# Kernel tuning notes

Measured on AMD Instinct MI355X. Metric: run time of the kernel, lower is better.

Reference implementation:

```python
import jax, jax.numpy as jnp
import numpy as np
from itertools import combinations

NUM_LAGS = 9
WINDOWS = 4
HIDDEN = 256
BS = 32768
EPS = 1e-5  # BatchNorm eps


def _mean_adj():
    # Reconstruct the fixed per-sample DGL graph from get_batch_graph and
    # fold mean-aggregation into a row-normalized dense 9x9 matrix
    # (duplicate edges across overlapping windows count with multiplicity,
    # exactly as DGL's mailbox mean does).
    edges = []
    for j in range(WINDOWS, NUM_LAGS + 1):
        t = list(range(j - WINDOWS, j))
        combs = list(combinations(t, 2))
        for e in combs[:-1]:  # code drops the last combination per window
            edges.append(e)
    edges.append((NUM_LAGS - 2, NUM_LAGS - 1))
    edges.append((NUM_LAGS - 1, 0))
    A = np.zeros((NUM_LAGS, NUM_LAGS), np.float32)
    for s, d in edges:
        A[d, s] += 1.0  # messages flow src -> dst
    deg = A.sum(axis=1, keepdims=True)
    return A / np.maximum(deg, 1.0)

_A = jnp.asarray(_mean_adj())  # [9, 9]


def setup_inputs() -> dict:
    key = jax.random.key(0)
    ks = jax.random.split(key, 12)
    H = HIDDEN
    s = lambda fan_in: 1.0 / np.sqrt(fan_in)
    return {
        "lags": jax.random.normal(ks[0], (BS, NUM_LAGS), jnp.float32),
        "weather": jax.random.normal(ks[1], (BS, NUM_LAGS, 8), jnp.float32),
        "W_l1": jax.random.normal(ks[2], (1, H), jnp.float32) * s(1),
        "b_l1": jnp.zeros((H,), jnp.float32),
        "g_bn": jnp.ones((H,), jnp.float32),
        "b_bn": jnp.zeros((H,), jnp.float32),
        "W_l2": jax.random.normal(ks[3], (H, H), jnp.float32) * s(H),
        "b_l2": jnp.zeros((H,), jnp.float32),
        "W_w1": jax.random.normal(ks[4], (8, H), jnp.float32) * s(8),
        "b_w1": jnp.zeros((H,), jnp.float32),
        "W_w2": jax.random.normal(ks[5], (H, H), jnp.float32) * s(H),
        "b_w2": jnp.zeros((H,), jnp.float32),
        "Wm1": jax.random.normal(ks[6], (2 * H, H), jnp.float32) * s(2 * H),
        "bm1": jnp.zeros((H,), jnp.float32),
        "Wm2": jax.random.normal(ks[7], (2 * H, H), jnp.float32) * s(2 * H),
        "bm2": jnp.zeros((H,), jnp.float32),
        "W_reg": jax.random.normal(ks[8], (NUM_LAGS * H, 1), jnp.float32) * s(NUM_LAGS * H),
        "b_reg": jnp.zeros((1,), jnp.float32),
    }


def reference(lags, weather, W_l1, b_l1, g_bn, b_bn, W_l2, b_l2,
              W_w1, b_w1, W_w2, b_w2, Wm1, bm1, Wm2, bm2, W_reg, b_reg):
    bs = lags.shape[0]
    # lags branch: Linear(1,H) -> tanh -> [dropout=id] -> eval BatchNorm -> Linear(H,H) -> tanh
    l = jnp.tanh(lags.reshape(-1, 1) @ W_l1 + b_l1)
    l = l * (g_bn / jnp.sqrt(1.0 + EPS)) + b_bn  # BN eval: running_mean=0, running_var=1
    l = jnp.tanh(l @ W_l2 + b_l2)
    # weather branch: Linear(8,H) -> tanh -> Linear(H,H) -> tanh
    w = jnp.tanh(weather.reshape(-1, 8) @ W_w1 + b_w1)
    w = jnp.tanh(w @ W_w2 + b_w2)
    l = l.reshape(bs, NUM_LAGS, -1)
    w = w.reshape(bs, NUM_LAGS, -1)
    # Two MGN layers: mean-aggregate neighbor l and w, concat, linear merge.
    for Wm, bm in ((Wm1, bm1), (Wm2, bm2)):
        ml = jnp.einsum('ds,bsh->bdh', _A, l)  # mean over mailbox 'l'
        mw = jnp.einsum('ds,bsh->bdh', _A, w)  # mean over mailbox 'w'
        l = jnp.concatenate([ml, mw], axis=-1) @ Wm + bm
        w = mw
    hg = l.reshape(bs, -1)  # [bs, 9*H]
    return hg @ W_reg + b_reg
```

## Files before the change

### kernel.cpp

```cpp
#include <hip/hip_runtime.h>

typedef __attribute__((ext_vector_type(8))) short short8;
typedef __attribute__((ext_vector_type(4))) float float4v;

#define NLAGS 9
#define HID 256
#define GSAMP 16
#define NTHREADS 512
#define SBUF_SHORTS (36864 + 256 + 288)

#define NK 2048
#define LUT_STRIDE 2056
#define SLO -8.0f
#define KINV 128.0f

union S8 { short8 v; unsigned short u[8]; };

__device__ __forceinline__ unsigned short f2b(float f) {
  union { float f; unsigned int i; } c; c.f = f;
  return (unsigned short)((c.i + 0x7FFFu + ((c.i >> 16) & 1u)) >> 16);
}
__device__ __forceinline__ float sane(float x) {
  return (__builtin_isfinite(x) && fabsf(x) < 1e30f) ? x : 0.0f;
}
__device__ __forceinline__ unsigned int pkbf16(float lo, float hi) {
  unsigned int r;
  asm("v_cvt_pk_bf16_f32 %0, %1, %2" : "=v"(r) : "v"(lo), "v"(hi));
  return r;
}
__device__ __forceinline__ float ftanh(float x) {
  float t = __expf(2.0f * x);
  return 1.0f - 2.0f * __builtin_amdgcn_rcpf(t + 1.0f);
}
__device__ __forceinline__ float4v mfma16(short8 a, short8 b, float4v c) {
  return __builtin_amdgcn_mfma_f32_16x16x32_bf16(a, b, c, 0, 0, 0);
}

__device__ __forceinline__ int tmC(int row, int c) {
  int base = ((row >> 4) * 8 + (c >> 2)) * 512 + (row & 15) * 32 + (c & 3) * 8;
  return base ^ ((((c >> 2) ^ (row >> 2)) & 3) << 4);
}
__device__ __forceinline__ int tmE(int row, int col) {
  int base = ((row >> 4) * 8 + (col >> 5)) * 512 + (row & 15) * 32 + (col & 31);
  return base ^ ((((col >> 5) ^ (row >> 2)) & 3) << 4);
}

#define A_TABLE { \
    {0,0,0,0,0,0,0,0,1}, \
    {1,0,0,0,0,0,0,0,0}, \
    {1.f/3,2.f/3,0,0,0,0,0,0,0}, \
    {0.2f,0.4f,0.4f,0,0,0,0,0,0}, \
    {0,0.2f,0.4f,0.4f,0,0,0,0,0}, \
    {0,0,0.2f,0.4f,0.4f,0,0,0,0}, \
    {0,0,0,0.2f,0.4f,0.4f,0,0,0}, \
    {0,0,0,0,0.25f,0.5f,0.25f,0,0}, \
    {0,0,0,0,0,1.f/3,1.f/3,1.f/3,0}, \
  }

__global__ void prep_all(const float* __restrict__ Ww2,
                         const float* __restrict__ Ww1,
                         const float* __restrict__ Wm2,
                         const float* __restrict__ Wreg,
                         const float* __restrict__ bm2,
                         const float* __restrict__ breg,
                         unsigned short* __restrict__ ws,
                         float* __restrict__ vtab)
{
  const int b = blockIdx.x;
  if (b < 144) {
    int idx = b * 512 + threadIdx.x + 65536;
    if (idx < 131072) {
      int j = idx - 65536; int n = j >> 8, k = j & 255;
      ws[idx] = f2b(sane(Ww2[k * 256 + n]));
    } else {
      int j = idx - 131072; int n = j >> 5, k = j & 31;
      ws[idx] = (k < 8) ? f2b(sane(Ww1[k * 256 + n])) : (unsigned short)0;
    }
    return;
  }
  const float A[9][9] = A_TABLE;
  const int lane = threadIdx.x & 63;
  const int g = (b - 144) * 8 + (threadIdx.x >> 6);
  if (g < 4608) {
    int mat = (g >= 2304);
    int w = g - mat * 2304;
    int d = w >> 8, k = w & 255;
    float coef[9];
    #pragma unroll
    for (int dp = 0; dp < 9; ++dp) {
      if (!mat) {
        coef[dp] = A[dp][d];
      } else {
        float s = 0.f;
        #pragma unroll
        for (int e = 0; e < 9; ++e) s += A[dp][e] * A[e][d];
        coef[dp] = s;
      }
    }
    const float* wm2row = Wm2 + (size_t)(mat * 256 + k) * 256;
    float acc = 0.f;
    #pragma unroll
    for (int it = 0; it < 4; ++it) {
      int h = lane + it * 64;
      float wp = 0.f;
      #pragma unroll
      for (int dp = 0; dp < 9; ++dp) wp = fmaf(coef[dp], Wreg[dp * 256 + h], wp);
      acc = fmaf(wp, wm2row[h], acc);
    }
    #pragma unroll
    for (int off = 32; off >= 1; off >>= 1) acc += __shfl_down(acc, off);
    if (lane == 0) vtab[5120 + g] = acc;
  } else if (g == 4608) {
    float c0 = 0.f;
    #pragma unroll
    for (int it = 0; it < 4; ++it) {
      int h = lane + it * 64;
      float cs = 0.f;
      #pragma unroll
      for (int d = 0; d < 9; ++d) cs += Wreg[d * 256 + h];
      c0 = fmaf(bm2[h], cs, c0);
    }
    #pragma unroll
    for (int off = 32; off >= 1; off >>= 1) c0 += __shfl_down(c0, off);
    if (lane == 0) vtab[9728] = c0 + breg[0];
  }
}

__global__ void prep2b_kernel(const float* __restrict__ Wm1,
                              const float* __restrict__ bm1,
                              float* __restrict__ vtab)
{
  const float A[9][9] = A_TABLE;
  const float* V1s = vtab + 5120;
  const float* V2s = vtab + 7424;
  const int lane = threadIdx.x & 63;
  const int g = blockIdx.x * 8 + (threadIdx.x >> 6);
  if (g < 4608) {
    int mat = (g >= 2304);
    int w = g - mat * 2304;
    int s = w >> 8, k = w & 255;
    const float* wm1row = Wm1 + (size_t)(mat * 256 + k) * 256;
    float acc = 0.f;
    #pragma unroll
    for (int it = 0; it < 4; ++it) {
      int h = lane + it * 64;
      float u = 0.f;
      #pragma unroll
      for (int d = 0; d < 9; ++d) u = fmaf(A[d][s], V1s[d * 256 + h], u);
      acc = fmaf(u, wm1row[h], acc);
    }
    #pragma unroll
    for (int off = 32; off >= 1; off >>= 1) acc += __shfl_down(acc, off);
    if (lane == 0) vtab[g] = acc + (mat ? V2s[s * 256 + k] : 0.f);
  } else if (g == 4608) {
    float c = 0.f;
    #pragma unroll
    for (int it = 0; it < 4; ++it) {
      int h = lane + it * 64;
      float vs = 0.f;
      #pragma unroll
      for (int d = 0; d < 9; ++d) vs += V1s[d * 256 + h];
      c = fmaf(bm1[h], vs, c);
    }
    #pragma unroll
    for (int off = 32; off >= 1; off >>= 1) c += __shfl_down(c, off);
    if (lane == 0) vtab[4608] = c + vtab[9728];
  }
}

__global__ void prep3_lut(const float* __restrict__ Wl1,
                          const float* __restrict__ bl1,
                          const float* __restrict__ gbn,
                          const float* __restrict__ bbn,
                          const float* __restrict__ Wl2,
                          const float* __restrict__ bl2,
                          const float* __restrict__ vtab,
                          float* __restrict__ lutf)
{
  __shared__ float l0s[2][256];
  __shared__ float red[2][9][4];
  const int tid = threadIdx.x;
  const int b = blockIdx.x;
  const float BNS = 0.99999500003750f;
  {
    float w = Wl1[tid], a = bl1[tid], g = gbn[tid] * BNS, q = bbn[tid];
    #pragma unroll
    for (int j = 0; j < 2; ++j) {
      float s = SLO + (float)(b * 2 + j) * 0.0078125f;
      l0s[j][tid] = fmaf(ftanh(fmaf(s, w, a)), g, q);
    }
  }
  __syncthreads();
  float z0 = bl2[tid], z1 = z0;
  #pragma unroll 8
  for (int k = 0; k < 256; ++k) {
    float wv = Wl2[k * 256 + tid];
    z0 = fmaf(l0s[0][k], wv, z0);
    z1 = fmaf(l0s[1][k], wv, z1);
  }
  float t0 = ftanh(z0), t1 = ftanh(z1);
  const int lane = tid & 63, w4 = tid >> 6;
  for (int d = 0; d < 9; ++d) {
    float T1h = vtab[d * 256 + tid];
    float v0 = t0 * T1h, v1 = t1 * T1h;
    #pragma unroll
    for (int off = 32; off >= 1; off >>= 1) {
      v0 += __shfl_down(v0, off);
      v1 += __shfl_down(v1, off);
    }
    if (lane == 0) { red[0][d][w4] = v0; red[1][d][w4] = v1; }
  }
  __syncthreads();
  if (tid < 18) {
    int j = tid / 9, d = tid - j * 9;
    float v = red[j][d][0] + red[j][d][1] + red[j][d][2] + red[j][d][3];
    lutf[d * LUT_STRIDE + (b * 2 + j)] = v;
  }
}

__global__ void __launch_bounds__(NTHREADS, 2)
fused_kernel(const float* __restrict__ lags,
             const float* __restrict__ weather,
             const float* __restrict__ bw1,
             const float* __restrict__ bw2,
             const unsigned short* __restrict__ ws,
             const float* __restrict__ vtab,
             float* __restrict__ out)
{
  __shared__ __align__(16) unsigned short sBuf[SBUF_SHORTS];
  unsigned short* sT = sBuf;
  float* scratch  = (float*)(sBuf + 36864);
  float* scratch2 = (float*)(sBuf + 36864 + 256);

  const int tid = threadIdx.x;
  const int wave = tid >> 6;
  const int lane16 = tid & 15;
  const int g4 = (tid >> 4) & 3;
  const int s0 = blockIdx.x * GSAMP;

  const float* lutf = (const float*)ws;
  const unsigned short* Ww2t = ws + 65536;
  const unsigned short* Ww1p = ws + 131072;

  const int c0 = wave * 32 + lane16;
  const int c1 = wave * 32 + 16 + lane16;

  if (tid < 144) {
    int samp = tid / 9, d = tid - samp * 9;
    float x = lags[(s0 + samp) * NLAGS + d];
    float tp = (x - SLO) * KINV;
    tp = fminf(fmaxf(tp, 0.0f), (float)(NK - 2) + 0.999f);
    int j = (int)tp; float fr = tp - (float)j;
    const float* row = lutf + d * LUT_STRIDE;
    float lo = row[j], hi = row[j + 1];
    scratch2[tid] = fmaf(fr, hi - lo, lo);
  }

  {
    short8 bf0 = *(const short8*)(Ww1p + c0 * 32 + g4 * 8);
    short8 bf1 = *(const short8*)(Ww1p + c1 * 32 + g4 * 8);
    float bia0 = bw1[c0], bia1 = bw1[c1];
    #pragma unroll
    for (int m = 0; m < 9; ++m) {
      S8 a8;
      if (g4 == 0) {
        const float* wp = weather + (size_t)(s0 + lane16) * 72 + m * 8;
        float4v x0 = *(const float4v*)(wp);
        float4v x1 = *(const float4v*)(wp + 4);
        a8.v = (short8){0,0,0,0,0,0,0,0};
        unsigned int p0 = pkbf16(x0[0], x0[1]), p1 = pkbf16(x0[2], x0[3]);
        unsigned int p2 = pkbf16(x1[0], x1[1]), p3 = pkbf16(x1[2], x1[3]);
        a8.u[0] = (unsigned short)p0; a8.u[1] = (unsigned short)(p0 >> 16);
        a8.u[2] = (unsigned short)p1; a8.u[3] = (unsigned short)(p1 >> 16);
        a8.u[4] = (unsigned short)p2; a8.u[5] = (unsigned short)(p2 >> 16);
        a8.u[6] = (unsigned short)p3; a8.u[7] = (unsigned short)(p3 >> 16);
      } else {
        a8.v = (short8){0,0,0,0,0,0,0,0};
      }
      float4v zz = {0.f, 0.f, 0.f, 0.f};
      float4v ac0 = mfma16(a8.v, bf0, zz);
      float4v ac1 = mfma16(a8.v, bf1, zz);
      #pragma unroll
      for (int i = 0; i < 4; ++i) {
        int row = m * 16 + g4 * 4 + i;
        unsigned int p = pkbf16(ftanh(ac0[i] + bia0), ftanh(ac1[i] + bia1));
        sT[tmE(row, c0)] = (unsigned short)p;
        sT[tmE(row, c1)] = (unsigned short)(p >> 16);
      }
    }
  }
  __syncthreads();

  float P[4] = {0.f, 0.f, 0.f, 0.f};

  {
    float4v acc0[9], acc1[9];
    #pragma unroll
    for (int m = 0; m < 9; ++m) {
      float4v z = {0.f,0.f,0.f,0.f};
      acc0[m] = z; acc1[m] = z;
    }
    #pragma unroll
    for (int kk = 0; kk < 8; ++kk) {
      short8 b0 = *(const short8*)(Ww2t + c0 * 256 + kk * 32 + g4 * 8);
      short8 b1 = *(const short8*)(Ww2t + c1 * 256 + kk * 32 + g4 * 8);
      #pragma unroll
      for (int m = 0; m < 9; ++m) {
        short8 a = *(const short8*)(sT + tmC(m * 16 + lane16, kk * 4 + g4));
        acc0[m] = mfma16(a, b0, acc0[m]);
        acc1[m] = mfma16(a, b1, acc1[m]);
      }
    }
    float twc0[9], twc1[9];
    #pragma unroll
    for (int m = 0; m < 9; ++m) {
      twc0[m] = vtab[2304 + m * 256 + c0];
      twc1[m] = vtab[2304 + m * 256 + c1];
    }
    float bia0 = bw2[c0], bia1 = bw2[c1];
    #pragma unroll
    for (int m = 0; m < 9; ++m) {
      #pragma unroll
      for (int i = 0; i < 4; ++i) {
        float t0 = ftanh(acc0[m][i] + bia0);
        float t1 = ftanh(acc1[m][i] + bia1);
        P[i] = fmaf(t0, twc0[m], P[i]);
        P[i] = fmaf(t1, twc1[m], P[i]);
      }
    }
  }

  #pragma unroll
  for (int off = 8; off >= 1; off >>= 1) {
    #pragma unroll
    for (int i = 0; i < 4; ++i) P[i] += __shfl_down(P[i], off, 16);
  }
  if (lane16 == 0) {
    #pragma unroll
    for (int i = 0; i < 4; ++i) scratch[wave * 16 + g4 * 4 + i] = P[i];
  }
  __syncthreads();
  if (tid < GSAMP) {
    float sum = 0.f;
    #pragma unroll
    for (int w = 0; w < 8; ++w) sum += scratch[w * 16 + tid];
    float lsum = 0.f;
    #pragma unroll
    for (int d = 0; d < 9; ++d) lsum += scratch2[tid * 9 + d];
    out[s0 + tid] = sum + lsum + vtab[4608];
  }
}

extern "C" void kernel_launch(void* const* d_in, const int* in_sizes, int n_in,
                              void* d_out, int out_size, void* d_ws, size_t ws_size,
                              hipStream_t stream) {
  const float* lags    = (const float*)d_in[0];
  const float* weather = (const float*)d_in[1];
  const float* Wl1     = (const float*)d_in[2];
  const float* bl1     = (const float*)d_in[3];
  const float* gbn     = (const float*)d_in[4];
  const float* bbn     = (const float*)d_in[5];
  const float* Wl2     = (const float*)d_in[6];
  const float* bl2     = (const float*)d_in[7];
  const float* Ww1     = (const float*)d_in[8];
  const float* bw1     = (const float*)d_in[9];
  const float* Ww2     = (const float*)d_in[10];
  const float* bw2     = (const float*)d_in[11];
  const float* Wm1     = (const float*)d_in[12];
  const float* bm1     = (const float*)d_in[13];
  const float* Wm2     = (const float*)d_in[14];
  const float* bm2     = (const float*)d_in[15];
  const float* Wreg    = (const float*)d_in[16];
  const float* breg    = (const float*)d_in[17];
  unsigned short* ws = (unsigned short*)d_ws;
  float* vtab = (float*)(ws + 139264);
  float* lutf = (float*)ws;

  prep_all<<<721, 512, 0, stream>>>(Ww2, Ww1, Wm2, Wreg, bm2, breg, ws, vtab);
  prep2b_kernel<<<577, 512, 0, stream>>>(Wm1, bm1, vtab);
  prep3_lut<<<1024, 256, 0, stream>>>(Wl1, bl1, gbn, bbn, Wl2, bl2, vtab, lutf);

  const int nblocks = 32768 / GSAMP;
  fused_kernel<<<nblocks, NTHREADS, 0, stream>>>(
      lags, weather, bw1, bw2, ws, vtab, (float*)d_out);
}
```

Baseline: 213.8 us.

## Merge two weight-prep kernels by folding Wm1·Wm2 product into one pass

Replaces the two dependent prep kernels (prep_all then prep2b) with a single prep_A kernel. Each wavefront computes a row of Wm1·Wm2 directly, then contracts it with the A² graph coefficients and W_reg to fill the nine vtab entries for that row. The bias constant is computed in the same launch. This removes one kernel launch and the global round trip of the intermediate V tables. In exchange each wave does a serial 256-step inner loop over Wm2 rows, which means more compute and memory traffic per wave on far fewer blocks.

```diff
diff --git a/kernel.cpp b/kernel.cpp
--- a/kernel.cpp
+++ b/kernel.cpp
@@ -57,18 +57,21 @@
     {0,0,0,0,0,1.f/3,1.f/3,1.f/3,0}, \
   }
 
-__global__ void prep_all(const float* __restrict__ Ww2,
-                         const float* __restrict__ Ww1,
-                         const float* __restrict__ Wm2,
-                         const float* __restrict__ Wreg,
-                         const float* __restrict__ bm2,
-                         const float* __restrict__ breg,
-                         unsigned short* __restrict__ ws,
-                         float* __restrict__ vtab)
+__global__ void prep_A(const float* __restrict__ Ww2,
+                       const float* __restrict__ Ww1,
+                       const float* __restrict__ Wm1,
+                       const float* __restrict__ Wm2,
+                       const float* __restrict__ Wreg,
+                       const float* __restrict__ bm1,
+                       const float* __restrict__ bm2,
+                       const float* __restrict__ breg,
+                       unsigned short* __restrict__ ws,
+                       float* __restrict__ vtab)
 {
   const int b = blockIdx.x;
+  const int tid = threadIdx.x;
   if (b < 144) {
-    int idx = b * 512 + threadIdx.x + 65536;
+    int idx = b * 512 + tid + 65536;
     if (idx < 131072) {
       int j = idx - 65536; int n = j >> 8, k = j & 255;
       ws[idx] = f2b(sane(Ww2[k * 256 + n]));
@@ -78,93 +81,101 @@
     }
     return;
   }
+  const int lane = tid & 63;
+  const int jw = (b - 144) * 8 + (tid >> 6);
   const float A[9][9] = A_TABLE;
-  const int lane = threadIdx.x & 63;
-  const int g = (b - 144) * 8 + (threadIdx.x >> 6);
-  if (g < 4608) {
-    int mat = (g >= 2304);
-    int w = g - mat * 2304;
-    int d = w >> 8, k = w & 255;
-    float coef[9];
+  float B[9][9];
+  #pragma unroll
+  for (int dp = 0; dp < 9; ++dp)
+    #pragma unroll
+    for (int s = 0; s < 9; ++s) {
+      float v = 0.f;
+      #pragma unroll
+      for (int e = 0; e < 9; ++e) v += A[dp][e] * A[e][s];
+      B[dp][s] = v;
+    }
+
+  if (jw < 512) {
+    const int mat = jw >> 8, k = jw & 255;
+    float m[4] = {0.f, 0.f, 0.f, 0.f};
+    const float* wm1row = Wm1 + (size_t)(mat * 256 + k) * 256;
+    #pragma unroll 4
+    for (int h = 0; h < 256; ++h) {
+      float w1v = wm1row[h];
+      const float* w2r = Wm2 + (size_t)h * 256;
+      #pragma unroll
+      for (int i = 0; i < 4; ++i) m[i] = fmaf(w1v, w2r[lane + i * 64], m[i]);
+    }
+    if (mat) {
+      const float* w2b = Wm2 + (size_t)(256 + k) * 256;
+      #pragma unroll
+      for (int i = 0; i < 4; ++i) m[i] += w2b[lane + i * 64];
+    }
+    float wr[9][4];
+    #pragma unroll
+    for (int dp = 0; dp < 9; ++dp)
+      #pragma unroll
+      for (int i = 0; i < 4; ++i) wr[dp][i] = Wreg[dp * 256 + lane + i * 64];
+    float acc9[9];
+    #pragma unroll
+    for (int s = 0; s < 9; ++s) {
+      float t = 0.f;
+      #pragma unroll
+      for (int i = 0; i < 4; ++i) {
+        float p2 = 0.f;
+        #pragma unroll
+        for (int dp = 0; dp < 9; ++dp) p2 = fmaf(B[dp][s], wr[dp][i], p2);
+        t = fmaf(p2, m[i], t);
+      }
+      acc9[s] = t;
+    }
+    #pragma unroll
+    for (int s = 0; s < 9; ++s) {
+      #pragma unroll
+      for (int off = 32; off >= 1; off >>= 1) acc9[s] += __shfl_down(acc9[s], off);
+    }
+    if (lane == 0) {
+      #pragma unroll
+      for (int s = 0; s < 9; ++s)
+        vtab[(mat ? 2304 : 0) + s * 256 + k] = acc9[s];
+    }
+  } else if (jw == 512) {
+    float rsum[9];
     #pragma unroll
     for (int dp = 0; dp < 9; ++dp) {
-      if (!mat) {
-        coef[dp] = A[dp][d];
-      } else {
-        float s = 0.f;
-        #pragma unroll
-        for (int e = 0; e < 9; ++e) s += A[dp][e] * A[e][d];
-        coef[dp] = s;
-      }
-    }
-    const float* wm2row = Wm2 + (size_t)(mat * 256 + k) * 256;
-    float acc = 0.f;
-    #pragma unroll
-    for (int it = 0; it < 4; ++it) {
-      int h = lane + it * 64;
-      float wp = 0.f;
-      #pragma unroll
-      for (int dp = 0; dp < 9; ++dp) wp = fmaf(coef[dp], Wreg[dp * 256 + h], wp);
-      acc = fmaf(wp, wm2row[h], acc);
-    }
-    #pragma unroll
-    for (int off = 32; off >= 1; off >>= 1) acc += __shfl_down(acc, off);
-    if (lane == 0) vtab[5120 + g] = acc;
-  } else if (g == 4608) {
-    float c0 = 0.f;
-    #pragma unroll
-    for (int it = 0; it < 4; ++it) {
-      int h = lane + it * 64;
-      float cs = 0.f;
-      #pragma unroll
-      for (int d = 0; d < 9; ++d) cs += Wreg[d * 256 + h];
-      c0 = fmaf(bm2[h], cs, c0);
-    }
-    #pragma unroll
-    for (int off = 32; off >= 1; off >>= 1) c0 += __shfl_down(c0, off);
-    if (lane == 0) vtab[9728] = c0 + breg[0];
-  }
-}
-
-__global__ void prep2b_kernel(const float* __restrict__ Wm1,
-                              const float* __restrict__ bm1,
-                              float* __restrict__ vtab)
-{
-  const float A[9][9] = A_TABLE;
-  const float* V1s = vtab + 5120;
-  const float* V2s = vtab + 7424;
-  const int lane = threadIdx.x & 63;
-  const int g = blockIdx.x * 8 + (threadIdx.x >> 6);
-  if (g < 4608) {
-    int mat = (g >= 2304);
-    int w = g - mat * 2304;
-    int s = w >> 8, k = w & 255;
-    const float* wm1row = Wm1 + (size_t)(mat * 256 + k) * 256;
-    float acc = 0.f;
-    #pragma unroll
-    for (int it = 0; it < 4; ++it) {
-      int h = lane + it * 64;
-      float u = 0.f;
-      #pragma unroll
-      for (int d = 0; d < 9; ++d) u = fmaf(A[d][s], V1s[d * 256 + h], u);
-      acc = fmaf(u, wm1row[h], acc);
-    }
-    #pragma unroll
-    for (int off = 32; off >= 1; off >>= 1) acc += __shfl_down(acc, off);
-    if (lane == 0) vtab[g] = acc + (mat ? V2s[s * 256 + k] : 0.f);
-  } else if (g == 4608) {
-    float c = 0.f;
-    #pragma unroll
-    for (int it = 0; it < 4; ++it) {
-      int h = lane + it * 64;
-      float vs = 0.f;
-      #pragma unroll
-      for (int d = 0; d < 9; ++d) vs += V1s[d * 256 + h];
-      c = fmaf(bm1[h], vs, c);
-    }
-    #pragma unroll
-    for (int off = 32; off >= 1; off >>= 1) c += __shfl_down(c, off);
-    if (lane == 0) vtab[4608] = c + vtab[9728];
+      float v = 0.f;
+      #pragma unroll
+      for (int d = 0; d < 9; ++d) v += A[dp][d];
+      rsum[dp] = v;
+    }
+    float R[4], part1 = 0.f;
+    #pragma unroll
+    for (int i = 0; i < 4; ++i) {
+      int h = lane + i * 64;
+      float r = 0.f, cs = 0.f;
+      #pragma unroll
+      for (int dp = 0; dp < 9; ++dp) {
+        float wv = Wreg[dp * 256 + h];
+        r = fmaf(rsum[dp], wv, r);
+        cs += wv;
+      }
+      R[i] = r;
+      part1 = fmaf(bm2[h], cs, part1);
+    }
+    float sb[4] = {0.f, 0.f, 0.f, 0.f};
+    #pragma unroll 4
+    for (int ho = 0; ho < 256; ++ho) {
+      float b1 = bm1[ho];
+      const float* w2r = Wm2 + (size_t)ho * 256;
+      #pragma unroll
+      for (int i = 0; i < 4; ++i) sb[i] = fmaf(b1, w2r[lane + i * 64], sb[i]);
+    }
+    float tot = part1;
+    #pragma unroll
+    for (int i = 0; i < 4; ++i) tot = fmaf(R[i], sb[i], tot);
+    #pragma unroll
+    for (int off = 32; off >= 1; off >>= 1) tot += __shfl_down(tot, off);
+    if (lane == 0) vtab[4608] = tot + breg[0];
   }
 }
 
@@ -376,8 +387,8 @@
   float* vtab = (float*)(ws + 139264);
   float* lutf = (float*)ws;
 
-  prep_all<<<721, 512, 0, stream>>>(Ww2, Ww1, Wm2, Wreg, bm2, breg, ws, vtab);
-  prep2b_kernel<<<577, 512, 0, stream>>>(Wm1, bm1, vtab);
+  prep_A<<<209, 512, 0, stream>>>(Ww2, Ww1, Wm1, Wm2, Wreg, bm1, bm2, breg,
+                                  ws, vtab);
   prep3_lut<<<1024, 256, 0, stream>>>(Wl1, bl1, gbn, bbn, Wl2, bl2, vtab, lutf);
 
   const int nblocks = 32768 / GSAMP;
```

Measured after the change: 228.2 us. +6.7%, slower.

## Double threads per block, one column tile per wave, chunk M loop

Applied to the files above, without the earlier changes.

Raises the block to 1024 threads so each wave owns a single 16-column tile instead of two, and splits the 9 row tiles of the second GEMM into three non-unrolled groups of three accumulators. This cuts accumulator registers per thread and adds more waves to hide latency. In exchange each wave now reloads the Ww2 B fragments three times (the asm barrier blocks hoisting them) and the A fragments are read twice as often across waves. The launch bounds min-blocks value of 2 with 1024 threads may also force tight register limits.

```diff
diff --git a/kernel.cpp b/kernel.cpp
--- a/kernel.cpp
+++ b/kernel.cpp
@@ -6,8 +6,8 @@
 #define NLAGS 9
 #define HID 256
 #define GSAMP 16
-#define NTHREADS 512
-#define SBUF_SHORTS (36864 + 256 + 288)
+#define NTHREADS 1024
+#define SBUF_SHORTS (36864 + 512 + 288)
 
 #define NK 2048
 #define LUT_STRIDE 2056
@@ -230,7 +230,7 @@
   __shared__ __align__(16) unsigned short sBuf[SBUF_SHORTS];
   unsigned short* sT = sBuf;
   float* scratch  = (float*)(sBuf + 36864);
-  float* scratch2 = (float*)(sBuf + 36864 + 256);
+  float* scratch2 = (float*)(sBuf + 36864 + 512);
 
   const int tid = threadIdx.x;
   const int wave = tid >> 6;
@@ -242,8 +242,7 @@
   const unsigned short* Ww2t = ws + 65536;
   const unsigned short* Ww1p = ws + 131072;
 
-  const int c0 = wave * 32 + lane16;
-  const int c1 = wave * 32 + 16 + lane16;
+  const int c = wave * 16 + lane16;
 
   if (tid < 144) {
     int samp = tid / 9, d = tid - samp * 9;
@@ -257,9 +256,8 @@
   }
 
   {
-    short8 bf0 = *(const short8*)(Ww1p + c0 * 32 + g4 * 8);
-    short8 bf1 = *(const short8*)(Ww1p + c1 * 32 + g4 * 8);
-    float bia0 = bw1[c0], bia1 = bw1[c1];
+    short8 bf = *(const short8*)(Ww1p + c * 32 + g4 * 8);
+    float bia = bw1[c];
     #pragma unroll
     for (int m = 0; m < 9; ++m) {
       S8 a8;
@@ -278,15 +276,16 @@
         a8.v = (short8){0,0,0,0,0,0,0,0};
       }
       float4v zz = {0.f, 0.f, 0.f, 0.f};
-      float4v ac0 = mfma16(a8.v, bf0, zz);
-      float4v ac1 = mfma16(a8.v, bf1, zz);
-      #pragma unroll
-      for (int i = 0; i < 4; ++i) {
-        int row = m * 16 + g4 * 4 + i;
-        unsigned int p = pkbf16(ftanh(ac0[i] + bia0), ftanh(ac1[i] + bia1));
-        sT[tmE(row, c0)] = (unsigned short)p;
-        sT[tmE(row, c1)] = (unsigned short)(p >> 16);
-      }
+      float4v ac = mfma16(a8.v, bf, zz);
+      float t0 = ftanh(ac[0] + bia), t1 = ftanh(ac[1] + bia);
+      float t2 = ftanh(ac[2] + bia), t3 = ftanh(ac[3] + bia);
+      unsigned int p01 = pkbf16(t0, t1);
+      unsigned int p23 = pkbf16(t2, t3);
+      int r0 = m * 16 + g4 * 4;
+      sT[tmE(r0 + 0, c)] = (unsigned short)p01;
+      sT[tmE(r0 + 1, c)] = (unsigned short)(p01 >> 16);
+      sT[tmE(r0 + 2, c)] = (unsigned short)p23;
+      sT[tmE(r0 + 3, c)] = (unsigned short)(p23 >> 16);
     }
   }
   __syncthreads();
@@ -294,38 +293,37 @@
   float P[4] = {0.f, 0.f, 0.f, 0.f};
 
   {
-    float4v acc0[9], acc1[9];
-    #pragma unroll
-    for (int m = 0; m < 9; ++m) {
-      float4v z = {0.f,0.f,0.f,0.f};
-      acc0[m] = z; acc1[m] = z;
-    }
-    #pragma unroll
-    for (int kk = 0; kk < 8; ++kk) {
-      short8 b0 = *(const short8*)(Ww2t + c0 * 256 + kk * 32 + g4 * 8);
-      short8 b1 = *(const short8*)(Ww2t + c1 * 256 + kk * 32 + g4 * 8);
-      #pragma unroll
-      for (int m = 0; m < 9; ++m) {
-        short8 a = *(const short8*)(sT + tmC(m * 16 + lane16, kk * 4 + g4));
-        acc0[m] = mfma16(a, b0, acc0[m]);
-        acc1[m] = mfma16(a, b1, acc1[m]);
-      }
-    }
-    float twc0[9], twc1[9];
-    #pragma unroll
-    for (int m = 0; m < 9; ++m) {
-      twc0[m] = vtab[2304 + m * 256 + c0];
-      twc1[m] = vtab[2304 + m * 256 + c1];
-    }
-    float bia0 = bw2[c0], bia1 = bw2[c1];
-    #pragma unroll
-    for (int m = 0; m < 9; ++m) {
-      #pragma unroll
-      for (int i = 0; i < 4; ++i) {
-        float t0 = ftanh(acc0[m][i] + bia0);
-        float t1 = ftanh(acc1[m][i] + bia1);
-        P[i] = fmaf(t0, twc0[m], P[i]);
-        P[i] = fmaf(t1, twc1[m], P[i]);
+    float bia = bw2[c];
+    #pragma unroll 1
+    for (int mg = 0; mg < 3; ++mg) {
+      int lz = 0;
+      asm volatile("" : "+v"(lz));
+      const unsigned short* Wb = Ww2t + lz;
+      float4v acc[3];
+      #pragma unroll
+      for (int mi = 0; mi < 3; ++mi) {
+        float4v z = {0.f,0.f,0.f,0.f};
+        acc[mi] = z;
+      }
+      #pragma unroll
+      for (int kk = 0; kk < 8; ++kk) {
+        short8 b0 = *(const short8*)(Wb + c * 256 + kk * 32 + g4 * 8);
+        #pragma unroll
+        for (int mi = 0; mi < 3; ++mi) {
+          int m = mg * 3 + mi;
+          short8 a = *(const short8*)(sT + tmC(m * 16 + lane16, kk * 4 + g4));
+          acc[mi] = mfma16(a, b0, acc[mi]);
+        }
+      }
+      #pragma unroll
+      for (int mi = 0; mi < 3; ++mi) {
+        int m = mg * 3 + mi;
+        float twc = vtab[2304 + m * 256 + c];
+        #pragma unroll
+        for (int i = 0; i < 4; ++i) {
+          float t0 = ftanh(acc[mi][i] + bia);
+          P[i] = fmaf(t0, twc, P[i]);
+        }
       }
     }
   }
@@ -343,7 +341,7 @@
   if (tid < GSAMP) {
     float sum = 0.f;
     #pragma unroll
-    for (int w = 0; w < 8; ++w) sum += scratch[w * 16 + tid];
+    for (int w = 0; w < 16; ++w) sum += scratch[w * 16 + tid];
     float lsum = 0.f;
     #pragma unroll
     for (int d = 0; d < 9; ++d) lsum += scratch2[tid * 9 + d];
```

New measurement: 233.6 us. +9.3%, slower.
